# Kernel tuning notes

Hardware: AMD Instinct MI355X
Metric: run time of the kernel (lower is better)

## Reference

```python
import jax, jax.numpy as jnp
import numpy as np

B, N = 65536, 8
OBS0, OBS1, OBS2 = 6, 1024, 7
H, HC, NA = 64, 128, 2


def _glorot(key, shape):
    fan_in = shape[0]
    lim = 1.0 / np.sqrt(fan_in)
    return jax.random.uniform(key, shape, jnp.float32, -lim, lim)


def setup_inputs() -> dict:
    key = jax.random.key(0)
    ks = jax.random.split(key, 24)
    state0 = jax.random.normal(ks[0], (B, OBS0), jnp.float32)
    state1 = jax.random.normal(ks[1], (B, OBS1), jnp.float32)
    state2 = jax.random.normal(ks[2], (B, N, OBS2), jnp.float32)
    keep = (jax.random.uniform(ks[3], (B, N, 1)) > 0.35) | (jnp.arange(N)[None, :, None] == 0)
    state2 = state2 * keep.astype(jnp.float32)
    return {
        "state0": state0, "state1": state1, "state2": state2,
        "W0": _glorot(ks[4], (OBS0, H)), "b0": jnp.zeros((H,), jnp.float32),
        "Wg": _glorot(ks[5], (OBS1, H)), "bg": jnp.zeros((H,), jnp.float32),
        "Ws1": _glorot(ks[6], (OBS2, H)), "bs1": jnp.zeros((H,), jnp.float32),
        "Ws2": _glorot(ks[7], (H, H)), "bs2": jnp.zeros((H,), jnp.float32),
        "Wq": _glorot(ks[8], (H, H)),
        "Wk": _glorot(ks[9], (H, H)),
        "Wv": _glorot(ks[10], (H, H)),
        "Wc1": _glorot(ks[11], (3 * H, HC)), "bc1": jnp.zeros((HC,), jnp.float32),
        "Wc2": _glorot(ks[12], (HC, HC)), "bc2": jnp.zeros((HC,), jnp.float32),
        "Wc3": _glorot(ks[13], (HC, NA)), "bc3": jnp.zeros((NA,), jnp.float32),
    }


def reference(state0, state1, state2,
              W0, b0, Wg, bg, Ws1, bs1, Ws2, bs2,
              Wq, Wk, Wv, Wc1, bc1, Wc2, bc2, Wc3, bc3):
    own_e = jax.nn.relu(state0 @ W0 + b0)                      # [B, 64]
    env_e = jax.nn.relu(state1 @ Wg + bg)                      # [B, 64]
    intru_e = jax.nn.relu(state2 @ Ws1 + bs1)                  # [B, N, 64]
    intru_e = jax.nn.relu(intru_e @ Ws2 + bs2)                 # [B, N, 64]

    q = own_e @ Wq                                             # [B, 64]
    k = intru_e @ Wk                                           # [B, N, 64]
    v = intru_e @ Wv                                           # [B, N, 64]

    # mask: True where the neighbor slot is non-padding (mean over feats != 0)
    mask = jnp.mean(state2, axis=2, keepdims=True) != 0        # [B, N, 1] bool

    score = jnp.einsum('bnd,bd->bn', k, q)[..., None]          # [B, N, 1]
    score_m = jnp.where(mask, score, -jnp.inf)
    alpha = jax.nn.softmax(score_m / np.sqrt(H), axis=1)       # [B, N, 1]
    alpha_m = jnp.where(mask, alpha, 0.0)
    v_att = jnp.sum(v * alpha_m, axis=1)                       # [B, 64]

    concat = jnp.concatenate((own_e, env_e, v_att), axis=1)    # [B, 192]
    h = jax.nn.relu(concat @ Wc1 + bc1)
    h = jax.nn.relu(h @ Wc2 + bc2)
    return jnp.tanh(h @ Wc3 + bc3)                             # [B, n_actions]
```

## Files before the change

kernel.cpp:

```cpp
#include <hip/hip_runtime.h>
#include <math.h>


typedef float f32x4 __attribute__((ext_vector_type(4)));
typedef float f32x4u __attribute__((ext_vector_type(4), aligned(4)));
typedef float f32x2u __attribute__((ext_vector_type(2), aligned(4)));
typedef __bf16 bf16x8 __attribute__((ext_vector_type(8)));
typedef unsigned short u16x8 __attribute__((ext_vector_type(8)));

#define DI __device__ __forceinline__

DI unsigned short f2bf_u(float f) {
  unsigned u = __builtin_bit_cast(unsigned, f);
  u += 0x7fffu + ((u >> 16) & 1u);
  return (unsigned short)(u >> 16);
}
DI float bfu2f(unsigned short s) {
  unsigned u = ((unsigned)s) << 16;
  return __builtin_bit_cast(float, u);
}
DI u16x8 cvt8(f32x4 x, f32x4 y) {
  bf16x8 r;
  r[0] = (__bf16)x[0]; r[1] = (__bf16)x[1]; r[2] = (__bf16)x[2]; r[3] = (__bf16)x[3];
  r[4] = (__bf16)y[0]; r[5] = (__bf16)y[1]; r[6] = (__bf16)y[2]; r[7] = (__bf16)y[3];
  return __builtin_bit_cast(u16x8, r);
}
DI f32x4 mfma16(u16x8 a, u16x8 b, f32x4 c) {
  return __builtin_amdgcn_mfma_f32_16x16x32_bf16(
      __builtin_bit_cast(bf16x8, a), __builtin_bit_cast(bf16x8, b), c, 0, 0, 0);
}
DI void gload_lds16(const void* g, void* l) {
  typedef __attribute__((address_space(1))) const unsigned GU;
  typedef __attribute__((address_space(3))) unsigned LU;
  __builtin_amdgcn_global_load_lds((GU*)g, (LU*)l, 16, 0, 0);
}


constexpr size_t WS_WGF = 0;
constexpr size_t WS_WS2 = 131072;
constexpr size_t WS_WV  = 139264;
constexpr size_t WS_MQK = 147456;
constexpr size_t WS_WC1 = 155648;
constexpr size_t WS_WC2 = 204800;
constexpr size_t WS_ENV = 237568;

__global__ __launch_bounds__(256) void k_prep(
    const float* __restrict__ Wg, const float* __restrict__ Ws2,
    const float* __restrict__ Wv, const float* __restrict__ Wq,
    const float* __restrict__ Wk, const float* __restrict__ Wc1,
    const float* __restrict__ Wc2,
    unsigned short* __restrict__ wgf, unsigned short* __restrict__ ws2f,
    unsigned short* __restrict__ wvf, unsigned short* __restrict__ mqkf,
    unsigned short* __restrict__ wc1f, unsigned short* __restrict__ wc2f) {
  const int idx = blockIdx.x * 256 + threadIdx.x;
  const float* src = nullptr;
  unsigned short* dst;
  int i, ntm, NC;
  bool is_mqk = false;
  if (idx < 65536)      { src = Wg;  dst = wgf;  i = idx;          ntm = 2; NC = 64;  }
  else if (idx < 69632) { src = Ws2; dst = ws2f; i = idx - 65536;  ntm = 2; NC = 64;  }
  else if (idx < 73728) { src = Wv;  dst = wvf;  i = idx - 69632;  ntm = 2; NC = 64;  }
  else if (idx < 77824) { is_mqk = true; dst = mqkf; i = idx - 73728; ntm = 2; NC = 64; }
  else if (idx < 102400){ src = Wc1; dst = wc1f; i = idx - 77824;  ntm = 3; NC = 128; }
  else                  { src = Wc2; dst = wc2f; i = idx - 102400; ntm = 3; NC = 128; }
  const int j = i & 7, ln = (i >> 3) & 63, t2 = i >> 9;
  const int nt = t2 & ((1 << ntm) - 1), kt = t2 >> ntm;
  const int k = kt * 32 + (ln >> 4) * 8 + j, n = nt * 16 + (ln & 15);
  float val;
  if (is_mqk) {
    const f32x4* qp = (const f32x4*)(Wq + k * 64);
    const f32x4* kp = (const f32x4*)(Wk + n * 64);
    float acc = 0.f;
#pragma unroll
    for (int d4 = 0; d4 < 16; ++d4) {
      const f32x4 a = qp[d4], b = kp[d4];
#pragma unroll
      for (int e = 0; e < 4; ++e) acc = fmaf(a[e], b[e], acc);
    }
    val = acc;
  } else {
    val = src[k * NC + n];
  }
  dst[i] = f2bf_u(val);
}

__global__ __launch_bounds__(256, 4) void k_env(
    const float* __restrict__ s1, const unsigned short* __restrict__ wgf,
    const float* __restrict__ bg, unsigned short* __restrict__ envf) {
  __shared__ __align__(16) char smem[36864];
  unsigned short* STGs = (unsigned short*)(smem + 32768);
  u16x8* STG = (u16x8*)(smem + 32768);

  const int tid = threadIdx.x;
  const int lane = tid & 63, wave = tid >> 6;
  const int lo = lane & 15, q = lane >> 4;
  const int bbase = blockIdx.x * 32;
  const int mt = wave & 1, ntb = wave >> 1;

  const char* s1b = (const char*)(s1 + (size_t)bbase * 1024);

  int srow[4], scol[4];
#pragma unroll
  for (int i = 0; i < 4; ++i) {
    const int T = (i * 256 + tid) * 16;
    srow[i] = T >> 9;
    scol[i] = (T & 511) ^ ((srow[i] & 7) << 4);
  }
  auto stage = [&](char* dst, int c) {
    const int srcb = c * 512;
#pragma unroll
    for (int i = 0; i < 4; ++i)
      gload_lds16(s1b + (size_t)srow[i] * 4096 + srcb + scol[i],
                  dst + (i * 256 + tid) * 16);
  };

  f32x4 acc0 = {}, acc1 = {};
  const int row = mt * 16 + lo;
  const int sw = (row & 7) << 4;
  const u16x8* wgfp = (const u16x8*)wgf + (ntb * 2) * 64 + lane;

  auto compute = [&](const char* src, int c) {
#pragma unroll
    for (int kt = 0; kt < 4; ++kt) {
      const int base = row * 512 + kt * 128 + q * 32;
      const f32x4 alo = *(const f32x4*)(src + (base ^ sw));
      const f32x4 ahi = *(const f32x4*)(src + ((base + 16) ^ sw));
      const int ktg = c * 4 + kt;
      const u16x8 b0 = wgfp[(ktg * 4 + 0) * 64];
      const u16x8 b1 = wgfp[(ktg * 4 + 1) * 64];
      const u16x8 af = cvt8(alo, ahi);
      acc0 = mfma16(af, b0, acc0);
      acc1 = mfma16(af, b1, acc1);
    }
  };

  stage(smem, 0);
  __syncthreads();
#pragma unroll
  for (int cc = 0; cc < 4; ++cc) {
    stage(smem + 16384, cc * 2 + 1);
    compute(smem, cc * 2);
    __syncthreads();
    if (cc < 3) stage(smem, cc * 2 + 2);
    compute(smem + 16384, cc * 2 + 1);
    __syncthreads();
  }

#pragma unroll
  for (int ni = 0; ni < 2; ++ni) {
    const f32x4 a = ni ? acc1 : acc0;
    const int h = (ntb * 2 + ni) * 16 + lo;
    const float bias = bg[h];
#pragma unroll
    for (int ri = 0; ri < 4; ++ri) {
      const float v = fmaxf(a[ri] + bias, 0.f);
      STGs[((mt * 2 + ntb) * 64 + ((((h >> 3) & 3) << 4) | (q * 4 + ri))) * 8 +
           (h & 7)] = f2bf_u(v);
    }
  }
  __syncthreads();
  const u16x8 v = STG[(mt * 2 + ntb) * 64 + lane];
  *((u16x8*)envf + ((size_t)((bbase >> 4) + mt) * 2 + ntb) * 64 + lane) = v;
}

__global__ __launch_bounds__(256, 3) void k_rest(
    const float* __restrict__ s0, const float* __restrict__ s2,
    const float* __restrict__ W0, const float* __restrict__ b0v,
    const float* __restrict__ Ws1, const float* __restrict__ bs1,
    const unsigned short* __restrict__ ws2f, const float* __restrict__ bs2,
    const unsigned short* __restrict__ wvf, const unsigned short* __restrict__ mqkf,
    const unsigned short* __restrict__ wc1f, const float* __restrict__ bc1,
    const unsigned short* __restrict__ wc2f, const float* __restrict__ bc2,
    const float* __restrict__ Wc3, const float* __restrict__ bc3,
    const unsigned short* __restrict__ envf,
    float* __restrict__ out) {
  __shared__ __align__(16) char smem[54272];
  u16x8* EF = (u16x8*)smem;
  unsigned short* EFs = (unsigned short*)smem;
  u16x8* H1F = (u16x8*)smem;
  unsigned short* H1Fs = (unsigned short*)smem;
  float* H2 = (float*)(smem + 8192);
  u16x8* CF = (u16x8*)(smem + 32768);
  float* QK = (float*)(smem + 45056);
  u16x8* SEF = (u16x8*)(smem + 45056);
  float* SC = (float*)(smem + 53248);

  const int tid = threadIdx.x;
  const int lane = tid & 63, wave = tid >> 6;
  const int lo = lane & 15, q = lane >> 4;
  const int bbase = blockIdx.x * 32;

  const int emt_ = wave >> 1, ekt = wave & 1;
  const u16x8 ev =
      *((const u16x8*)envf + ((size_t)((bbase >> 4) + emt_) * 2 + ekt) * 64 + lane);

  const int bl8 = tid >> 3, n8 = tid & 7;
  const float* s2p = s2 + ((size_t)(bbase + bl8) * 8 + n8) * 7;
  const f32x4u x03 = *(const f32x4u*)s2p;
  const f32x2u x45 = *(const f32x2u*)(s2p + 4);
  const float x6 = s2p[6];
  const float* s0p = s0 + (size_t)(bbase + bl8) * 6;
  const f32x4u y03 = *(const f32x4u*)s0p;
  const f32x2u y45 = *(const f32x2u*)(s0p + 4);

  CF[(emt_ * 6 + 2 + ekt) * 64 + lane] = ev;

  bool maskreg;
  {
    float xv[7] = {x03[0], x03[1], x03[2], x03[3], x45[0], x45[1], x6};
    const float sum = xv[0] + xv[1] + xv[2] + xv[3] + xv[4] + xv[5] + xv[6];
    maskreg = (sum != 0.f);
    const int mt = tid >> 4, rl = tid & 15;
#pragma unroll
    for (int c = 0; c < 8; ++c) {
      float a[8];
#pragma unroll
      for (int i = 0; i < 8; ++i) a[i] = bs1[c * 8 + i];
#pragma unroll
      for (int j = 0; j < 7; ++j) {
        const float* wr = Ws1 + j * 64 + c * 8;
#pragma unroll
        for (int i = 0; i < 8; ++i) a[i] = fmaf(xv[j], wr[i], a[i]);
      }
      u16x8 pk;
#pragma unroll
      for (int i = 0; i < 8; ++i) pk[i] = f2bf_u(fmaxf(a[i], 0.f));
      EF[(mt * 2 + (c >> 2)) * 64 + (((c & 3) << 4) | rl)] = pk;
    }
  }
  __syncthreads();

  {
    u16x8 Bf[4][2];
#pragma unroll
    for (int nt = 0; nt < 4; ++nt)
#pragma unroll
      for (int kt = 0; kt < 2; ++kt)
        Bf[nt][kt] = ((const u16x8*)ws2f)[(kt * 4 + nt) * 64 + lane];
    float bias[4];
#pragma unroll
    for (int nt = 0; nt < 4; ++nt) bias[nt] = bs2[nt * 16 + lo];
#pragma unroll
    for (int mi = 0; mi < 4; ++mi) {
      const int mt = wave * 4 + mi;
      const u16x8 A0 = EF[(mt * 2 + 0) * 64 + lane];
      const u16x8 A1 = EF[(mt * 2 + 1) * 64 + lane];
      f32x4 acc[4] = {};
#pragma unroll
      for (int nt = 0; nt < 4; ++nt) {
        acc[nt] = mfma16(A0, Bf[nt][0], acc[nt]);
        acc[nt] = mfma16(A1, Bf[nt][1], acc[nt]);
      }
#pragma unroll
      for (int nt = 0; nt < 4; ++nt) {
        const int h = nt * 16 + lo;
#pragma unroll
        for (int ri = 0; ri < 4; ++ri) {
          const float v = fmaxf(acc[nt][ri] + bias[nt], 0.f);
          const int rr = mt * 16 + q * 4 + ri;
          EFs[((mt * 2 + (h >> 5)) * 64 + ((((h >> 3) & 3) << 4) | (rr & 15))) * 8 +
              (h & 7)] = f2bf_u(v);
        }
      }
    }
  }
  __syncthreads();

  {
    const int mt = bl8 >> 4, fl = ((n8 & 3) << 4) | (bl8 & 15), kt = n8 >> 2;
    const float yv[6] = {y03[0], y03[1], y03[2], y03[3], y45[0], y45[1]};
    float a[8];
#pragma unroll
    for (int i = 0; i < 8; ++i) a[i] = b0v[n8 * 8 + i];
#pragma unroll
    for (int j = 0; j < 6; ++j) {
      const float* wr = W0 + j * 64 + n8 * 8;
#pragma unroll
      for (int i = 0; i < 8; ++i) a[i] = fmaf(yv[j], wr[i], a[i]);
    }
    u16x8 pk;
#pragma unroll
    for (int i = 0; i < 8; ++i) pk[i] = f2bf_u(fmaxf(a[i], 0.f));
    CF[(mt * 6 + kt) * 64 + fl] = pk;
  }
  __syncthreads();

  {
#pragma unroll
    for (int pp = 0; pp < 2; ++pp) {
      const int pr = wave * 2 + pp, mt = pr >> 2, nt = pr & 3;
      const u16x8 A0 = CF[(mt * 6 + 0) * 64 + lane];
      const u16x8 A1 = CF[(mt * 6 + 1) * 64 + lane];
      const u16x8 B0 = ((const u16x8*)mqkf)[(0 * 4 + nt) * 64 + lane];
      const u16x8 B1 = ((const u16x8*)mqkf)[(1 * 4 + nt) * 64 + lane];
      f32x4 acc = {};
      acc = mfma16(A0, B0, acc);
      acc = mfma16(A1, B1, acc);
#pragma unroll
      for (int ri = 0; ri < 4; ++ri)
        QK[(mt * 16 + q * 4 + ri) * 64 + nt * 16 + lo] = acc[ri];
    }
  }
  __syncthreads();

  {
    const int r = tid, bl = r >> 3, mt = r >> 4, rl = r & 15;
    float dot = 0.f;
#pragma unroll
    for (int c = 0; c < 8; ++c) {
      const u16x8 e = EF[(mt * 2 + (c >> 2)) * 64 + (((c & 3) << 4) | rl)];
      const float* qkp = QK + bl * 64 + c * 8;
      const f32x4 qa = *(const f32x4*)(qkp);
      const f32x4 qb = *(const f32x4*)(qkp + 4);
#pragma unroll
      for (int i = 0; i < 4; ++i) dot = fmaf(bfu2f(e[i]), qa[i], dot);
#pragma unroll
      for (int i = 0; i < 4; ++i) dot = fmaf(bfu2f(e[4 + i]), qb[i], dot);
    }
    SC[r] = maskreg ? dot * 0.125f : -1e30f;
  }
  __syncthreads();

  if (tid < 32) {
    float s[8];
#pragma unroll
    for (int n = 0; n < 8; ++n) s[n] = SC[tid * 8 + n];
    float mx = s[0];
#pragma unroll
    for (int n = 1; n < 8; ++n) mx = fmaxf(mx, s[n]);
    float e[8], sum = 0.f;
#pragma unroll
    for (int n = 0; n < 8; ++n) { e[n] = __expf(s[n] - mx); sum += e[n]; }
    const float inv = 1.f / sum;
#pragma unroll
    for (int n = 0; n < 8; ++n) SC[tid * 8 + n] = e[n] * inv;
  }
  __syncthreads();

  {
    float al[8];
#pragma unroll
    for (int n = 0; n < 8; ++n) al[n] = SC[bl8 * 8 + n];
    float a[8] = {0.f, 0.f, 0.f, 0.f, 0.f, 0.f, 0.f, 0.f};
#pragma unroll
    for (int n = 0; n < 8; ++n) {
      const int rr = bl8 * 8 + n;
      const u16x8 e =
          EF[((rr >> 4) * 2 + (n8 >> 2)) * 64 + (((n8 & 3) << 4) | (rr & 15))];
#pragma unroll
      for (int i = 0; i < 8; ++i) a[i] = fmaf(al[n], bfu2f(e[i]), a[i]);
    }
    u16x8 pk;
#pragma unroll
    for (int i = 0; i < 8; ++i) pk[i] = f2bf_u(a[i]);
    SEF[((bl8 >> 4) * 2 + (n8 >> 2)) * 64 + (((n8 & 3) << 4) | (bl8 & 15))] = pk;
  }
  __syncthreads();

  {
    unsigned short* CFs = (unsigned short*)CF;
#pragma unroll
    for (int pp = 0; pp < 2; ++pp) {
      const int pr = wave * 2 + pp, mt = pr >> 2, nt = pr & 3;
      const u16x8 A0 = SEF[(mt * 2 + 0) * 64 + lane];
      const u16x8 A1 = SEF[(mt * 2 + 1) * 64 + lane];
      const u16x8 B0 = ((const u16x8*)wvf)[(0 * 4 + nt) * 64 + lane];
      const u16x8 B1 = ((const u16x8*)wvf)[(1 * 4 + nt) * 64 + lane];
      f32x4 acc = {};
      acc = mfma16(A0, B0, acc);
      acc = mfma16(A1, B1, acc);
      const int h = nt * 16 + lo;
#pragma unroll
      for (int ri = 0; ri < 4; ++ri) {
        const int rr = mt * 16 + q * 4 + ri;
        CFs[((mt * 6 + 4 + (h >> 5)) * 64 + ((((h >> 3) & 3) << 4) | (rr & 15))) * 8 +
            (h & 7)] = f2bf_u(acc[ri]);
      }
    }
  }
  __syncthreads();

  {
    const int mt = wave & 1, ntb = (wave >> 1) * 4;
    u16x8 A[6];
#pragma unroll
    for (int kt = 0; kt < 6; ++kt) A[kt] = CF[(mt * 6 + kt) * 64 + lane];
#pragma unroll
    for (int ni = 0; ni < 4; ++ni) {
      const int nt = ntb + ni;
      f32x4 acc = {};
#pragma unroll
      for (int kt = 0; kt < 6; ++kt) {
        const u16x8 Bf = ((const u16x8*)wc1f)[(kt * 8 + nt) * 64 + lane];
        acc = mfma16(A[kt], Bf, acc);
      }
      const float bias = bc1[nt * 16 + lo];
      const int h = nt * 16 + lo;
#pragma unroll
      for (int ri = 0; ri < 4; ++ri) {
        const float v = fmaxf(acc[ri] + bias, 0.f);
        const int rr = mt * 16 + q * 4 + ri;
        H1Fs[((mt * 4 + (h >> 5)) * 64 + ((((h >> 3) & 3) << 4) | (rr & 15))) * 8 +
             (h & 7)] = f2bf_u(v);
      }
    }
  }
  __syncthreads();

  {
    const int mt = wave & 1, ntb = (wave >> 1) * 4;
    u16x8 A[4];
#pragma unroll
    for (int kt = 0; kt < 4; ++kt) A[kt] = H1F[(mt * 4 + kt) * 64 + lane];
#pragma unroll
    for (int ni = 0; ni < 4; ++ni) {
      const int nt = ntb + ni;
      f32x4 acc = {};
#pragma unroll
      for (int kt = 0; kt < 4; ++kt) {
        const u16x8 Bf = ((const u16x8*)wc2f)[(kt * 8 + nt) * 64 + lane];
        acc = mfma16(A[kt], Bf, acc);
      }
      const float bias = bc2[nt * 16 + lo];
#pragma unroll
      for (int ri = 0; ri < 4; ++ri)
        H2[(mt * 16 + q * 4 + ri) * 132 + nt * 16 + lo] =
            fmaxf(acc[ri] + bias, 0.f);
    }
  }
  __syncthreads();

  {
    const int kq = n8 >> 1, a = n8 & 1;
    const f32x4* h4 = (const f32x4*)(H2 + bl8 * 132 + kq * 32);
    const float* wr = Wc3 + kq * 64;
    float acc = 0.f;
#pragma unroll
    for (int j4 = 0; j4 < 8; ++j4) {
      const f32x4 hv = h4[j4];
#pragma unroll
      for (int e = 0; e < 4; ++e) acc = fmaf(hv[e], wr[(j4 * 4 + e) * 2 + a], acc);
    }
    acc += __shfl_down(acc, 2);
    acc += __shfl_down(acc, 4);
    if (kq == 0) out[(size_t)(bbase + bl8) * 2 + a] = tanhf(acc + bc3[a]);
  }
}

extern "C" void kernel_launch(void* const* d_in, const int* in_sizes, int n_in,
                              void* d_out, int out_size, void* d_ws, size_t ws_size,
                              hipStream_t stream) {
  const float* s0  = (const float*)d_in[0];
  const float* s1  = (const float*)d_in[1];
  const float* s2  = (const float*)d_in[2];
  const float* W0  = (const float*)d_in[3];
  const float* b0  = (const float*)d_in[4];
  const float* Wg  = (const float*)d_in[5];
  const float* bg  = (const float*)d_in[6];
  const float* Ws1 = (const float*)d_in[7];
  const float* bs1 = (const float*)d_in[8];
  const float* Ws2 = (const float*)d_in[9];
  const float* bs2 = (const float*)d_in[10];
  const float* Wq  = (const float*)d_in[11];
  const float* Wk  = (const float*)d_in[12];
  const float* Wv  = (const float*)d_in[13];
  const float* Wc1 = (const float*)d_in[14];
  const float* bc1 = (const float*)d_in[15];
  const float* Wc2 = (const float*)d_in[16];
  const float* bc2 = (const float*)d_in[17];
  const float* Wc3 = (const float*)d_in[18];
  const float* bc3 = (const float*)d_in[19];

  char* ws = (char*)d_ws;
  unsigned short* wgf  = (unsigned short*)(ws + WS_WGF);
  unsigned short* ws2f = (unsigned short*)(ws + WS_WS2);
  unsigned short* wvf  = (unsigned short*)(ws + WS_WV);
  unsigned short* mqkf = (unsigned short*)(ws + WS_MQK);
  unsigned short* wc1f = (unsigned short*)(ws + WS_WC1);
  unsigned short* wc2f = (unsigned short*)(ws + WS_WC2);
  unsigned short* envf = (unsigned short*)(ws + WS_ENV);

  hipLaunchKernelGGL(k_prep, dim3(464), dim3(256), 0, stream, Wg, Ws2, Wv, Wq,
                     Wk, Wc1, Wc2, wgf, ws2f, wvf, mqkf, wc1f, wc2f);
  hipLaunchKernelGGL(k_env, dim3(2048), dim3(256), 0, stream, s1, wgf, bg, envf);
  hipLaunchKernelGGL(k_rest, dim3(2048), dim3(256), 0, stream, s0, s2, W0, b0,
                     Ws1, bs1, ws2f, bs2, wvf, mqkf, wc1f, bc1, wc2f, bc2, Wc3,
                     bc3, envf, (float*)d_out);
}
```

Baseline: 470.7 us.

## Fuse env-embedding GEMM into main kernel, dropping the intermediate buffer

Moves the state1 @ Wg MFMA stage, with its double-buffered global-to-LDS staging, into the main per-batch kernel. Its bf16 output now goes straight into the concat LDS tile instead of a global workspace buffer. This removes one kernel launch and the global write and re-read of the env embedding. The cost is that the large state1 stream now runs at the main kernel's lower occupancy and larger LDS footprint, and can no longer overlap with another kernel.

New measurement: 453.4 us. -3.7%, faster.

```diff
diff --git a/kernel.cpp b/kernel.cpp
--- a/kernel.cpp
+++ b/kernel.cpp
@@ -42,7 +42,6 @@
 constexpr size_t WS_MQK = 147456;
 constexpr size_t WS_WC1 = 155648;
 constexpr size_t WS_WC2 = 204800;
-constexpr size_t WS_ENV = 237568;
 
 __global__ __launch_bounds__(256) void k_prep(
     const float* __restrict__ Wg, const float* __restrict__ Ws2,
@@ -84,95 +83,17 @@
   dst[i] = f2bf_u(val);
 }
 
-__global__ __launch_bounds__(256, 4) void k_env(
-    const float* __restrict__ s1, const unsigned short* __restrict__ wgf,
-    const float* __restrict__ bg, unsigned short* __restrict__ envf) {
-  __shared__ __align__(16) char smem[36864];
-  unsigned short* STGs = (unsigned short*)(smem + 32768);
-  u16x8* STG = (u16x8*)(smem + 32768);
-
-  const int tid = threadIdx.x;
-  const int lane = tid & 63, wave = tid >> 6;
-  const int lo = lane & 15, q = lane >> 4;
-  const int bbase = blockIdx.x * 32;
-  const int mt = wave & 1, ntb = wave >> 1;
-
-  const char* s1b = (const char*)(s1 + (size_t)bbase * 1024);
-
-  int srow[4], scol[4];
-#pragma unroll
-  for (int i = 0; i < 4; ++i) {
-    const int T = (i * 256 + tid) * 16;
-    srow[i] = T >> 9;
-    scol[i] = (T & 511) ^ ((srow[i] & 7) << 4);
-  }
-  auto stage = [&](char* dst, int c) {
-    const int srcb = c * 512;
-#pragma unroll
-    for (int i = 0; i < 4; ++i)
-      gload_lds16(s1b + (size_t)srow[i] * 4096 + srcb + scol[i],
-                  dst + (i * 256 + tid) * 16);
-  };
-
-  f32x4 acc0 = {}, acc1 = {};
-  const int row = mt * 16 + lo;
-  const int sw = (row & 7) << 4;
-  const u16x8* wgfp = (const u16x8*)wgf + (ntb * 2) * 64 + lane;
-
-  auto compute = [&](const char* src, int c) {
-#pragma unroll
-    for (int kt = 0; kt < 4; ++kt) {
-      const int base = row * 512 + kt * 128 + q * 32;
-      const f32x4 alo = *(const f32x4*)(src + (base ^ sw));
-      const f32x4 ahi = *(const f32x4*)(src + ((base + 16) ^ sw));
-      const int ktg = c * 4 + kt;
-      const u16x8 b0 = wgfp[(ktg * 4 + 0) * 64];
-      const u16x8 b1 = wgfp[(ktg * 4 + 1) * 64];
-      const u16x8 af = cvt8(alo, ahi);
-      acc0 = mfma16(af, b0, acc0);
-      acc1 = mfma16(af, b1, acc1);
-    }
-  };
-
-  stage(smem, 0);
-  __syncthreads();
-#pragma unroll
-  for (int cc = 0; cc < 4; ++cc) {
-    stage(smem + 16384, cc * 2 + 1);
-    compute(smem, cc * 2);
-    __syncthreads();
-    if (cc < 3) stage(smem, cc * 2 + 2);
-    compute(smem + 16384, cc * 2 + 1);
-    __syncthreads();
-  }
-
-#pragma unroll
-  for (int ni = 0; ni < 2; ++ni) {
-    const f32x4 a = ni ? acc1 : acc0;
-    const int h = (ntb * 2 + ni) * 16 + lo;
-    const float bias = bg[h];
-#pragma unroll
-    for (int ri = 0; ri < 4; ++ri) {
-      const float v = fmaxf(a[ri] + bias, 0.f);
-      STGs[((mt * 2 + ntb) * 64 + ((((h >> 3) & 3) << 4) | (q * 4 + ri))) * 8 +
-           (h & 7)] = f2bf_u(v);
-    }
-  }
-  __syncthreads();
-  const u16x8 v = STG[(mt * 2 + ntb) * 64 + lane];
-  *((u16x8*)envf + ((size_t)((bbase >> 4) + mt) * 2 + ntb) * 64 + lane) = v;
-}
-
-__global__ __launch_bounds__(256, 3) void k_rest(
-    const float* __restrict__ s0, const float* __restrict__ s2,
+__global__ __launch_bounds__(256, 3) void k_main(
+    const float* __restrict__ s0, const float* __restrict__ s1,
+    const float* __restrict__ s2,
     const float* __restrict__ W0, const float* __restrict__ b0v,
+    const unsigned short* __restrict__ wgf, const float* __restrict__ bg,
     const float* __restrict__ Ws1, const float* __restrict__ bs1,
     const unsigned short* __restrict__ ws2f, const float* __restrict__ bs2,
     const unsigned short* __restrict__ wvf, const unsigned short* __restrict__ mqkf,
     const unsigned short* __restrict__ wc1f, const float* __restrict__ bc1,
     const unsigned short* __restrict__ wc2f, const float* __restrict__ bc2,
     const float* __restrict__ Wc3, const float* __restrict__ bc3,
-    const unsigned short* __restrict__ envf,
     float* __restrict__ out) {
   __shared__ __align__(16) char smem[54272];
   u16x8* EF = (u16x8*)smem;
@@ -181,6 +102,7 @@
   unsigned short* H1Fs = (unsigned short*)smem;
   float* H2 = (float*)(smem + 8192);
   u16x8* CF = (u16x8*)(smem + 32768);
+  unsigned short* CFs = (unsigned short*)(smem + 32768);
   float* QK = (float*)(smem + 45056);
   u16x8* SEF = (u16x8*)(smem + 45056);
   float* SC = (float*)(smem + 53248);
@@ -189,10 +111,6 @@
   const int lane = tid & 63, wave = tid >> 6;
   const int lo = lane & 15, q = lane >> 4;
   const int bbase = blockIdx.x * 32;
-
-  const int emt_ = wave >> 1, ekt = wave & 1;
-  const u16x8 ev =
-      *((const u16x8*)envf + ((size_t)((bbase >> 4) + emt_) * 2 + ekt) * 64 + lane);
 
   const int bl8 = tid >> 3, n8 = tid & 7;
   const float* s2p = s2 + ((size_t)(bbase + bl8) * 8 + n8) * 7;
@@ -203,7 +121,70 @@
   const f32x4u y03 = *(const f32x4u*)s0p;
   const f32x2u y45 = *(const f32x2u*)(s0p + 4);
 
-  CF[(emt_ * 6 + 2 + ekt) * 64 + lane] = ev;
+  {
+    const int mt = wave & 1, ntb = wave >> 1;
+    const char* s1b = (const char*)(s1 + (size_t)bbase * 1024);
+
+    int srow[4], scol[4];
+#pragma unroll
+    for (int i = 0; i < 4; ++i) {
+      const int T = (i * 256 + tid) * 16;
+      srow[i] = T >> 9;
+      scol[i] = (T & 511) ^ ((srow[i] & 7) << 4);
+    }
+    auto stage = [&](char* dst, int c) {
+      const int srcb = c * 512;
+#pragma unroll
+      for (int i = 0; i < 4; ++i)
+        gload_lds16(s1b + (size_t)srow[i] * 4096 + srcb + scol[i],
+                    dst + (i * 256 + tid) * 16);
+    };
+
+    f32x4 acc0 = {}, acc1 = {};
+    const int row = mt * 16 + lo;
+    const int sw = (row & 7) << 4;
+    const u16x8* wgfp = (const u16x8*)wgf + (ntb * 2) * 64 + lane;
+
+    auto compute = [&](const char* src, int c) {
+#pragma unroll
+      for (int kt = 0; kt < 4; ++kt) {
+        const int base = row * 512 + kt * 128 + q * 32;
+        const f32x4 alo = *(const f32x4*)(src + (base ^ sw));
+        const f32x4 ahi = *(const f32x4*)(src + ((base + 16) ^ sw));
+        const int ktg = c * 4 + kt;
+        const u16x8 b0 = wgfp[(ktg * 4 + 0) * 64];
+        const u16x8 b1 = wgfp[(ktg * 4 + 1) * 64];
+        const u16x8 af = cvt8(alo, ahi);
+        acc0 = mfma16(af, b0, acc0);
+        acc1 = mfma16(af, b1, acc1);
+      }
+    };
+
+    stage(smem, 0);
+    __syncthreads();
+#pragma unroll
+    for (int cc = 0; cc < 4; ++cc) {
+      stage(smem + 16384, cc * 2 + 1);
+      compute(smem, cc * 2);
+      __syncthreads();
+      if (cc < 3) stage(smem, cc * 2 + 2);
+      compute(smem + 16384, cc * 2 + 1);
+      __syncthreads();
+    }
+
+#pragma unroll
+    for (int ni = 0; ni < 2; ++ni) {
+      const f32x4 a = ni ? acc1 : acc0;
+      const int h = (ntb * 2 + ni) * 16 + lo;
+      const float bias = bg[h];
+#pragma unroll
+      for (int ri = 0; ri < 4; ++ri) {
+        const float v = fmaxf(a[ri] + bias, 0.f);
+        CFs[((mt * 6 + 2 + (h >> 5)) * 64 +
+             ((((h >> 3) & 3) << 4) | (q * 4 + ri))) * 8 + (h & 7)] = f2bf_u(v);
+      }
+    }
+  }
 
   bool maskreg;
   {
@@ -358,7 +339,6 @@
   __syncthreads();
 
   {
-    unsigned short* CFs = (unsigned short*)CF;
 #pragma unroll
     for (int pp = 0; pp < 2; ++pp) {
       const int pr = wave * 2 + pp, mt = pr >> 2, nt = pr & 3;
@@ -478,12 +458,10 @@
   unsigned short* mqkf = (unsigned short*)(ws + WS_MQK);
   unsigned short* wc1f = (unsigned short*)(ws + WS_WC1);
   unsigned short* wc2f = (unsigned short*)(ws + WS_WC2);
-  unsigned short* envf = (unsigned short*)(ws + WS_ENV);
 
   hipLaunchKernelGGL(k_prep, dim3(464), dim3(256), 0, stream, Wg, Ws2, Wv, Wq,
                      Wk, Wc1, Wc2, wgf, ws2f, wvf, mqkf, wc1f, wc2f);
-  hipLaunchKernelGGL(k_env, dim3(2048), dim3(256), 0, stream, s1, wgf, bg, envf);
-  hipLaunchKernelGGL(k_rest, dim3(2048), dim3(256), 0, stream, s0, s2, W0, b0,
-                     Ws1, bs1, ws2f, bs2, wvf, mqkf, wc1f, bc1, wc2f, bc2, Wc3,
-                     bc3, envf, (float*)d_out);
-}
+  hipLaunchKernelGGL(k_main, dim3(2048), dim3(256), 0, stream, s0, s1, s2, W0,
+                     b0, wgf, bg, Ws1, bs1, ws2f, bs2, wvf, mqkf, wc1f, bc1,
+                     wc2f, bc2, Wc3, bc3, (float*)d_out);
+}
```
